# Kernel tuning notes

Hardware: AMD Instinct MI355X
Metric: run time of the kernel (lower is better)

## Reference

```python
import jax, jax.numpy as jnp
import numpy as np

B, T, C, H = 2, 2048, 1024, 16
D = C // H
CURV = 1.0  # clamp_curvature(1.0) -> 1.0
EPS = 1e-5


def layer_norm(x, w, b):
    mu = jnp.mean(x, axis=-1, keepdims=True)
    var = jnp.var(x, axis=-1, keepdims=True)
    return (x - mu) * jax.lax.rsqrt(var + EPS) * w + b


def mobius_addition(x, y, c):
    xn2 = jnp.sum(x * x, axis=-1, keepdims=True)
    yn2 = jnp.sum(y * y, axis=-1, keepdims=True)
    ip = jnp.sum(x * y, axis=-1, keepdims=True)
    num = (1 + 2 * c * ip + c * yn2) * x + (1 - c * xn2) * y
    den = 1 + 2 * c * ip + (c ** 2) * xn2 * yn2
    return num / den


def scaling_factor(x, c):
    xn2 = jnp.sum(x * x, axis=-1, keepdims=True)
    return 2.0 / (1.0 + c * xn2)


def expmap(x, v, c):
    lam = scaling_factor(x, c)
    vn = jnp.linalg.norm(v, axis=-1, keepdims=True)
    second = (1.0 / c ** 0.5) * jnp.tanh(jnp.sqrt(c * lam * vn ** 2 / 2.0)) * v / vn
    return mobius_addition(x, second, c)


def logmap(x, u, c):
    lam = scaling_factor(x, c)
    m = mobius_addition(-x, u, c)
    mn = jnp.linalg.norm(m, axis=-1, keepdims=True)
    cf = 2.0 / (lam * c ** 0.5)
    arg = jnp.clip(jnp.sqrt(c * mn), -0.999, 0.999)
    return cf * jnp.arctanh(arg) * m / mn


def calc_reference_point(x):
    # shift-right by one token, zero at position 0
    return jnp.pad(x[:, :-1, :], ((0, 0), (1, 0), (0, 0)))


def causal_attention(q, k, v):
    # q,k,v: [B,H,T,D]
    scores = jnp.einsum('bhqd,bhkd->bhqk', q, k) / np.sqrt(D).astype(np.float32)
    mask = jnp.tril(jnp.ones((T, T), dtype=bool))
    scores = jnp.where(mask, scores, -jnp.inf)
    att = jax.nn.softmax(scores, axis=-1)
    return jnp.einsum('bhqk,bhkd->bhqd', att, v)


def setup_inputs() -> dict:
    key = jax.random.key(0)
    ks = jax.random.split(key, 6)
    s = 0.02
    return {
        'x': jax.random.normal(ks[0], (B, T, C), jnp.float32),
        'ln1_w': jnp.ones((C,), jnp.float32),
        'ln1_b': jnp.zeros((C,), jnp.float32),
        'W_attn': jax.random.normal(ks[1], (C, 3 * C), jnp.float32) * s,
        'b_attn': jnp.zeros((3 * C,), jnp.float32),
        'W_aproj': jax.random.normal(ks[2], (C, C), jnp.float32) * s,
        'b_aproj': jnp.zeros((C,), jnp.float32),
        'ln2_w': jnp.ones((C,), jnp.float32),
        'ln2_b': jnp.zeros((C,), jnp.float32),
        'W_fc': jax.random.normal(ks[3], (C, 4 * C), jnp.float32) * s,
        'b_fc': jnp.zeros((4 * C,), jnp.float32),
        'W_mproj': jax.random.normal(ks[4], (4 * C, C), jnp.float32) * s,
        'b_mproj': jnp.zeros((C,), jnp.float32),
    }


def reference(x, ln1_w, ln1_b, W_attn, b_attn, W_aproj, b_aproj,
              ln2_w, ln2_b, W_fc, b_fc, W_mproj, b_mproj):
    c = CURV
    # --- attention branch ---
    xn = layer_norm(x, ln1_w, ln1_b)
    ref = calc_reference_point(xn)
    xt = logmap(ref, xn, c)
    qkv = xt @ W_attn + b_attn
    q, k, v = jnp.split(qkv, 3, axis=-1)
    q = q.reshape(B, T, H, D).transpose(0, 2, 1, 3)
    k = k.reshape(B, T, H, D).transpose(0, 2, 1, 3)
    v = v.reshape(B, T, H, D).transpose(0, 2, 1, 3)
    y = causal_attention(q, k, v)
    y = y.transpose(0, 2, 1, 3).reshape(B, T, C)
    y = expmap(ref, y, c)  # map_back_after_attention=True
    y = y @ W_aproj + b_aproj
    x = x + y
    # --- MLP branch (no expmap since map_back_after_attention) ---
    h = layer_norm(x, ln2_w, ln2_b)
    h = jax.nn.gelu(h @ W_fc + b_fc, approximate=False)
    h = h @ W_mproj + b_mproj
    return x + h
```

## Files before the change

### kernel.cpp

```cpp
#include <hip/hip_runtime.h>
#include <hip/hip_bf16.h>
#include <math.h>

#define BDIM 2
#define TSEQ 2048
#define CDIM 1024
#define HNUM 16
#define NROW (BDIM*TSEQ)

typedef __attribute__((ext_vector_type(8))) short bf16x8_t;
typedef __attribute__((ext_vector_type(4))) float f32x4_t;

__device__ inline float bf2f(__hip_bfloat16 h) { return __bfloat162float(h); }

__device__ inline void unpack8(uint4 u, float* f) {
  unsigned v[4] = {u.x, u.y, u.z, u.w};
  #pragma unroll
  for (int i = 0; i < 4; ++i) {
    union { unsigned u2; float f2; } a, b;
    a.u2 = v[i] << 16;
    b.u2 = v[i] & 0xffff0000u;
    f[2*i]   = a.f2;
    f[2*i+1] = b.f2;
  }
}

__device__ inline void gload16(const void* g, void* l) {
  __builtin_amdgcn_global_load_lds(
      (const __attribute__((address_space(1))) void*)g,
      (__attribute__((address_space(3))) void*)l, 16, 0, 0);
}

__global__ __launch_bounds__(256) void zero32_kernel(float* p, int n) {
  int i = blockIdx.x * 256 + threadIdx.x;
  if (i < n) p[i] = 0.f;
}

__global__ __launch_bounds__(256) void convT_kernel(const float* __restrict__ src,
    __hip_bfloat16* __restrict__ dst, int K, int N)
{
  __shared__ float tile[32][33];
  const int k0 = blockIdx.x * 32, n0 = blockIdx.y * 32;
  const int tr  = threadIdx.x >> 3;
  const int tc4 = (threadIdx.x & 7) * 4;
  float4 v = *(const float4*)(src + (size_t)(k0 + tr) * N + n0 + tc4);
  tile[tr][tc4+0] = v.x; tile[tr][tc4+1] = v.y;
  tile[tr][tc4+2] = v.z; tile[tr][tc4+3] = v.w;
  __syncthreads();
  union { ushort4 u; __hip_bfloat16 h[4]; } o;
  #pragma unroll
  for (int j = 0; j < 4; ++j) o.h[j] = __float2bfloat16(tile[tc4+j][tr]);
  *(ushort4*)(dst + (size_t)(n0 + tr) * K + k0 + tc4) = o.u;
}

__device__ inline void blk_reduce3(float& a, float& b, float& c, float* red) {
  const int lane = threadIdx.x & 63, wv = threadIdx.x >> 6;
  #pragma unroll
  for (int off = 32; off; off >>= 1) {
    a += __shfl_xor(a, off); b += __shfl_xor(b, off); c += __shfl_xor(c, off);
  }
  if (lane == 0) { red[wv] = a; red[4+wv] = b; red[8+wv] = c; }
  __syncthreads();
  a = red[0]+red[1]+red[2]+red[3];
  b = red[4]+red[5]+red[6]+red[7];
  c = red[8]+red[9]+red[10]+red[11];
}

__global__ __launch_bounds__(256) void ln_kernel(const float* __restrict__ x,
    const float* __restrict__ w, const float* __restrict__ b,
    __hip_bfloat16* __restrict__ out)
{
  const int row = blockIdx.x;
  const size_t base = (size_t)row * CDIM;
  const int lane = threadIdx.x & 63, wv = threadIdx.x >> 6;
  float v[4]; float s = 0.f, s2 = 0.f;
  #pragma unroll
  for (int k = 0; k < 4; ++k) {
    int d = threadIdx.x + k*256;
    float xe = x[base + d];
    v[k] = xe; s += xe; s2 += xe*xe;
  }
  __shared__ float red[8];
  #pragma unroll
  for (int off = 32; off; off >>= 1) { s += __shfl_xor(s, off); s2 += __shfl_xor(s2, off); }
  if (lane == 0) { red[wv] = s; red[4+wv] = s2; }
  __syncthreads();
  s  = red[0]+red[1]+red[2]+red[3];
  s2 = red[4]+red[5]+red[6]+red[7];
  float mu = s * (1.0f/CDIM);
  float var = s2 * (1.0f/CDIM) - mu*mu;
  float rstd = rsqrtf(fmaxf(var, 0.f) + 1e-5f);
  #pragma unroll
  for (int k = 0; k < 4; ++k) {
    int d = threadIdx.x + k*256;
    out[base + d] = __float2bfloat16((v[k]-mu)*rstd*w[d] + b[d]);
  }
}

__global__ __launch_bounds__(256) void scal1_kernel(const __hip_bfloat16* __restrict__ xn,
                                                    float2* __restrict__ pq)
{
  const int row = blockIdx.x;
  const bool has = (row & (TSEQ-1)) != 0;
  const __hip_bfloat16* u  = xn + (size_t)row * CDIM;
  const __hip_bfloat16* xp = xn + (size_t)(has ? row-1 : row) * CDIM;
  float sxx = 0.f, suu = 0.f, sxu = 0.f;
  #pragma unroll
  for (int k = 0; k < 4; ++k) {
    int d = threadIdx.x + k*256;
    float ue = bf2f(u[d]);
    float xe = has ? bf2f(xp[d]) : 0.f;
    sxx += xe*xe; suu += ue*ue; sxu += xe*ue;
  }
  __shared__ float red[12];
  blk_reduce3(sxx, suu, sxu, red);
  float den = 1.f - 2.f*sxu + sxx*suu;
  float inv = 1.f / fmaxf(den, 1e-30f);
  float cb = 1.f - sxx;
  float ca = 1.f - 2.f*sxu + suu;
  float mm = inv*inv*(cb*cb*suu - 2.f*ca*cb*sxu + ca*ca*sxx);
  float mn = sqrtf(fmaxf(mm, 0.f));
  float arg = fminf(sqrtf(mn), 0.999f);
  float fac = (1.f + sxx) * atanhf(arg) / fmaxf(mn, 1e-30f);
  if (threadIdx.x == 0)
    pq[row] = make_float2(fac*cb*inv, has ? -fac*ca*inv : 0.f);
}

__global__ __launch_bounds__(256) void scal2_kernel(const __hip_bfloat16* __restrict__ xn,
                                                    const __hip_bfloat16* __restrict__ y,
                                                    float2* __restrict__ sr)
{
  const int row = blockIdx.x;
  const bool has = (row & (TSEQ-1)) != 0;
  const __hip_bfloat16* xp = xn + (size_t)(has ? row-1 : row) * CDIM;
  const __hip_bfloat16* vr = y + (size_t)row * CDIM;
  float sxx = 0.f, svv = 0.f, sxv = 0.f;
  #pragma unroll
  for (int k = 0; k < 4; ++k) {
    int d = threadIdx.x + k*256;
    float ve = bf2f(vr[d]);
    float xe = has ? bf2f(xp[d]) : 0.f;
    sxx += xe*xe; svv += ve*ve; sxv += xe*ve;
  }
  __shared__ float red[12];
  blk_reduce3(sxx, svv, sxv, red);
  float lam = 2.f / (1.f + sxx);
  float vn  = sqrtf(fmaxf(svv, 1e-30f));
  float th  = tanhf(vn * sqrtf(0.5f*lam));
  float s   = th / vn;
  float yn2 = th*th;
  float ip  = s * sxv;
  float den = 1.f + 2.f*ip + sxx*yn2;
  float inv = 1.f / fmaxf(den, 1e-30f);
  if (threadIdx.x == 0)
    sr[row] = make_float2((1.f - sxx)*s*inv, has ? (1.f + 2.f*ip + yn2)*inv : 0.f);
}

__global__ __launch_bounds__(256) void mix_kernel(const __hip_bfloat16* __restrict__ in1,
    const __hip_bfloat16* __restrict__ in2, const float2* __restrict__ coef,
    __hip_bfloat16* __restrict__ out)
{
  const int r = blockIdx.x*2 + (threadIdx.x >> 7);
  const int d = (threadIdx.x & 127) * 8;
  const bool has = (r & (TSEQ-1)) != 0;
  const int rp = has ? r-1 : r;
  float2 c = coef[r];
  uint4 u1 = *(const uint4*)(in1 + (size_t)r*CDIM + d);
  uint4 u2 = *(const uint4*)(in2 + (size_t)rp*CDIM + d);
  float f1[8], f2[8];
  unpack8(u1, f1); unpack8(u2, f2);
  union { uint4 u; __hip_bfloat16 h[8]; } o;
  #pragma unroll
  for (int j = 0; j < 8; ++j) o.h[j] = __float2bfloat16(c.x*f1[j] + c.y*f2[j]);
  *(uint4*)(out + (size_t)r*CDIM + d) = o.u;
}

template<int BM, int BN, int MODE>
__global__ __launch_bounds__(256) void gemmT_kernel(
    const __hip_bfloat16* __restrict__ A, int lda,
    const __hip_bfloat16* __restrict__ Bt, int ldb,
    const float* __restrict__ bias,
    const float* __restrict__ res,
    void* __restrict__ outp,
    int N, int K)
{
  __shared__ __align__(16) __hip_bfloat16 As[BM*32];
  __shared__ __align__(16) __hip_bfloat16 Bs[BN*32];
  const int bm = blockIdx.x, bn = blockIdx.y;
  const int tid = threadIdx.x, lane = tid & 63, wv = tid >> 6;
  constexpr int FM = BM/32, FN = BN/32;
  const int wm = (wv >> 1) * (BM/2), wn = (wv & 1) * (BN/2);
  f32x4_t acc[FM][FN];
  #pragma unroll
  for (int m = 0; m < FM; ++m)
    #pragma unroll
    for (int n = 0; n < FN; ++n) acc[m][n] = (f32x4_t){0.f,0.f,0.f,0.f};

  const int fr = lane & 15, quad = lane >> 4, q8 = quad * 8;
  const int srow = lane >> 2, scol = (lane & 3) * 8;
  constexpr int SA = BM/16, SB = BN/16;
  const __hip_bfloat16* Ag = A  + (size_t)(bm*BM + srow)*lda + scol;
  const __hip_bfloat16* Bg = Bt + (size_t)(bn*BN + srow)*ldb + scol;

  for (int k0 = 0; k0 < K; k0 += 32) {
    __syncthreads();
    #pragma unroll
    for (int i = 0; i < SA/4; ++i) {
      int s = wv*(SA/4) + i;
      gload16(Ag + (size_t)(s*16)*lda + k0, &As[s*512]);
    }
    #pragma unroll
    for (int i = 0; i < SB/4; ++i) {
      int s = wv*(SB/4) + i;
      gload16(Bg + (size_t)(s*16)*ldb + k0, &Bs[s*512]);
    }
    __syncthreads();
    bf16x8_t af[FM], bfr[FN];
    #pragma unroll
    for (int m = 0; m < FM; ++m) af[m]  = *(const bf16x8_t*)&As[(wm + m*16 + fr)*32 + q8];
    #pragma unroll
    for (int n = 0; n < FN; ++n) bfr[n] = *(const bf16x8_t*)&Bs[(wn + n*16 + fr)*32 + q8];
    #pragma unroll
    for (int m = 0; m < FM; ++m)
      #pragma unroll
      for (int n = 0; n < FN; ++n)
        acc[m][n] = __builtin_amdgcn_mfma_f32_16x16x32_bf16(af[m], bfr[n], acc[m][n], 0, 0, 0);
  }

  #pragma unroll
  for (int m = 0; m < FM; ++m)
  #pragma unroll
  for (int n = 0; n < FN; ++n)
  #pragma unroll
  for (int r = 0; r < 4; ++r) {
    int row = bm*BM + wm + m*16 + quad*4 + r;
    int col = bn*BN + wn + n*16 + fr;
    size_t idx = (size_t)row * N + col;
    float v = acc[m][n][r];
    if (MODE == 0) {
      v += bias[col];
      ((__hip_bfloat16*)outp)[idx] = __float2bfloat16(v);
    } else if (MODE == 1) {
      v += bias[col] + res[idx];
      ((float*)outp)[idx] = v;
    } else if (MODE == 2) {
      v += bias[col];
      v = 0.5f * v * (1.0f + erff(v * 0.70710678118654752f));
      ((__hip_bfloat16*)outp)[idx] = __float2bfloat16(v);
    } else if (MODE == 5) {
      v += res[idx];
      ((float*)outp)[idx] = v;
    } else {
      v += res[idx];
      ((float*)outp)[idx] = v;
    }
  }
}

__device__ inline __hip_bfloat16* slot_ptr(__hip_bfloat16* p0, __hip_bfloat16* p1, int s) {
  return (s < 2048) ? p0 + (size_t)s*4096 : p1 + (size_t)(s-2048)*4096;
}

__global__ __launch_bounds__(256) void attn_kernel(const __hip_bfloat16* __restrict__ qkv,
                                                   __hip_bfloat16* __restrict__ y,
                                                   __hip_bfloat16* __restrict__ pO0,
                                                   __hip_bfloat16* __restrict__ pO1,
                                                   float2* __restrict__ ml)
{
  const int wid = blockIdx.x;
  int qt, ci;
  if (wid < 32)      { qt = 31 - (wid >> 2); ci = wid & 3; }
  else if (wid < 56) { int w = wid - 32; qt = 23 - w/3; ci = w - (23 - qt)*3; }
  else if (wid < 72) { int w = wid - 56; qt = 15 - (w >> 1); ci = w & 1; }
  else               { qt = 79 - wid; ci = 0; }
  const int tb = ci * 8;
  const int te = min(tb + 8, qt + 1);
  const bool direct = (qt < 8);

  const int pair = blockIdx.y;
  const int b  = pair >> 4;
  const int h  = pair & 15;
  const int tid = threadIdx.x;
  const int lane = tid & 63;
  const int wv = tid >> 6;
  const int t0 = qt * 64;

  __shared__ __align__(16) __hip_bfloat16 Ks[64*72];
  __shared__ __align__(16) __hip_bfloat16 Vt[64*72];
  __shared__ __align__(16) __hip_bfloat16 Ps[4][16*72];

  const int colq = lane & 15, quad = lane >> 4;
  const int q8 = quad * 8;

  const __hip_bfloat16* qp = qkv + ((size_t)(b*TSEQ + t0 + wv*16 + colq))*(3*CDIM) + h*64;
  const bf16x8_t qa0 = *(const bf16x8_t*)(qp + q8);
  const bf16x8_t qa1 = *(const bf16x8_t*)(qp + 32 + q8);

  f32x4_t oacc[4];
  #pragma unroll
  for (int tn = 0; tn < 4; ++tn) oacc[tn] = (f32x4_t){0.f,0.f,0.f,0.f};
  float mr[4] = {-1e30f,-1e30f,-1e30f,-1e30f};
  float lr[4] = {0.f,0.f,0.f,0.f};

  const int jr = tid >> 2;
  const int sg = (tid & 3) * 16;
  const size_t kvbase = ((size_t)(b*TSEQ))*(3*CDIM) + h*64;

  uint4 ck0, ck1, cv0, cv1;
  {
    const __hip_bfloat16* kp = qkv + kvbase + (size_t)(tb*64 + jr)*(3*CDIM) + CDIM + sg;
    ck0 = *(const uint4*)(kp);
    ck1 = *(const uint4*)(kp + 8);
    cv0 = *(const uint4*)(kp + CDIM);
    cv1 = *(const uint4*)(kp + CDIM + 8);
  }
  uint4 nk0 = ck0, nk1 = ck1, nv0 = cv0, nv1 = cv1;

  for (int t = tb; t < te; ++t) {
    __syncthreads();
    {
      *(uint4*)(&Ks[jr*72 + sg])     = ck0;
      *(uint4*)(&Ks[jr*72 + sg + 8]) = ck1;
      union { uint4 u; __hip_bfloat16 hh[8]; } a0, a1;
      a0.u = cv0; a1.u = cv1;
      #pragma unroll
      for (int e = 0; e < 8; ++e) Vt[(sg + e)*72 + jr]     = a0.hh[e];
      #pragma unroll
      for (int e = 0; e < 8; ++e) Vt[(sg + 8 + e)*72 + jr] = a1.hh[e];
    }
    if (t + 1 < te) {
      const __hip_bfloat16* kp = qkv + kvbase + (size_t)((t+1)*64 + jr)*(3*CDIM) + CDIM + sg;
      nk0 = *(const uint4*)(kp);
      nk1 = *(const uint4*)(kp + 8);
      nv0 = *(const uint4*)(kp + CDIM);
      nv1 = *(const uint4*)(kp + CDIM + 8);
    }
    __syncthreads();

    f32x4_t sacc[4];
    #pragma unroll
    for (int tn = 0; tn < 4; ++tn) {
      sacc[tn] = (f32x4_t){0.f,0.f,0.f,0.f};
      bf16x8_t bk0 = *(const bf16x8_t*)(&Ks[(tn*16 + colq)*72 + q8]);
      sacc[tn] = __builtin_amdgcn_mfma_f32_16x16x32_bf16(qa0, bk0, sacc[tn], 0, 0, 0);
      bf16x8_t bk1 = *(const bf16x8_t*)(&Ks[(tn*16 + colq)*72 + 32 + q8]);
      sacc[tn] = __builtin_amdgcn_mfma_f32_16x16x32_bf16(qa1, bk1, sacc[tn], 0, 0, 0);
    }

    float sc[4][4];
    #pragma unroll
    for (int tn = 0; tn < 4; ++tn)
    #pragma unroll
    for (int r = 0; r < 4; ++r) sc[tn][r] = sacc[tn][r] * 0.125f;
    if (t == qt) {
      #pragma unroll
      for (int tn = 0; tn < 4; ++tn)
      #pragma unroll
      for (int r = 0; r < 4; ++r) {
        int key = t*64 + tn*16 + colq;
        int row = t0 + wv*16 + quad*4 + r;
        if (key > row) sc[tn][r] = -1e30f;
      }
    }

    float mx[4];
    #pragma unroll
    for (int r = 0; r < 4; ++r) {
      mx[r] = fmaxf(fmaxf(sc[0][r], sc[1][r]), fmaxf(sc[2][r], sc[3][r]));
      #pragma unroll
      for (int off = 8; off; off >>= 1) mx[r] = fmaxf(mx[r], __shfl_xor(mx[r], off));
    }
    float al[4];
    #pragma unroll
    for (int r = 0; r < 4; ++r) {
      float mn = fmaxf(mr[r], mx[r]);
      al[r] = __expf(mr[r] - mn);
      mr[r] = mn;
    }
    float psum[4] = {0.f,0.f,0.f,0.f};
    #pragma unroll
    for (int tn = 0; tn < 4; ++tn)
    #pragma unroll
    for (int r = 0; r < 4; ++r) {
      float p = __expf(sc[tn][r] - mr[r]);
      psum[r] += p;
      Ps[wv][(quad*4 + r)*72 + tn*16 + colq] = __float2bfloat16(p);
    }
    #pragma unroll
    for (int r = 0; r < 4; ++r) {
      #pragma unroll
      for (int off = 8; off; off >>= 1) psum[r] += __shfl_xor(psum[r], off);
      lr[r] = lr[r]*al[r] + psum[r];
    }
    #pragma unroll
    for (int tn = 0; tn < 4; ++tn)
    #pragma unroll
    for (int r = 0; r < 4; ++r) oacc[tn][r] *= al[r];

    bf16x8_t pa0 = *(const bf16x8_t*)(&Ps[wv][colq*72 + q8]);
    bf16x8_t pa1 = *(const bf16x8_t*)(&Ps[wv][colq*72 + 32 + q8]);
    #pragma unroll
    for (int tn = 0; tn < 4; ++tn) {
      bf16x8_t vb0 = *(const bf16x8_t*)(&Vt[(tn*16 + colq)*72 + q8]);
      oacc[tn] = __builtin_amdgcn_mfma_f32_16x16x32_bf16(pa0, vb0, oacc[tn], 0, 0, 0);
      bf16x8_t vb1 = *(const bf16x8_t*)(&Vt[(tn*16 + colq)*72 + 32 + q8]);
      oacc[tn] = __builtin_amdgcn_mfma_f32_16x16x32_bf16(pa1, vb1, oacc[tn], 0, 0, 0);
    }

    ck0 = nk0; ck1 = nk1; cv0 = nv0; cv1 = nv1;
  }

  if (direct) {
    __hip_bfloat16* yp = y + ((size_t)(b*TSEQ + t0 + wv*16))*CDIM + h*64;
    #pragma unroll
    for (int tn = 0; tn < 4; ++tn)
    #pragma unroll
    for (int r = 0; r < 4; ++r) {
      yp[(size_t)(quad*4 + r)*CDIM + tn*16 + colq] = __float2bfloat16(oacc[tn][r] / lr[r]);
    }
  } else {
    int off = (qt >= 24) ? 40 + (qt-24)*4 : (qt >= 16) ? 16 + (qt-16)*3 : (qt-8)*2;
    int s = pair*72 + off + ci;
    __hip_bfloat16* op = slot_ptr(pO0, pO1, s);
    #pragma unroll
    for (int tn = 0; tn < 4; ++tn)
    #pragma unroll
    for (int r = 0; r < 4; ++r) {
      op[wv*1024 + tn*256 + r*64 + lane] = __float2bfloat16(oacc[tn][r]);
    }
    if (colq == 0) {
      #pragma unroll
      for (int r = 0; r < 4; ++r)
        ml[(size_t)s*64 + wv*16 + quad*4 + r] = make_float2(mr[r], lr[r]);
    }
  }
}

__global__ __launch_bounds__(256) void combine_kernel(__hip_bfloat16* __restrict__ pO0,
                                                      __hip_bfloat16* __restrict__ pO1,
                                                      const float2* __restrict__ ml,
                                                      __hip_bfloat16* __restrict__ y)
{
  const int qt = 8 + blockIdx.x;
  const int pair = blockIdx.y;
  const int b = pair >> 4, h = pair & 15;
  const int nch = (qt >= 24) ? 4 : (qt >= 16) ? 3 : 2;
  const int off = (qt >= 24) ? 40 + (qt-24)*4 : (qt >= 16) ? 16 + (qt-16)*3 : (qt-8)*2;
  const int s0 = pair*72 + off;
  const int tid = threadIdx.x;
  const int q = tid >> 2;
  const int dseg = (tid & 3) * 16;

  float mi[4], li[4];
  float M = -1e30f;
  #pragma unroll
  for (int i = 0; i < 4; ++i) {
    if (i < nch) {
      float2 t = ml[(size_t)(s0+i)*64 + q];
      mi[i] = t.x; li[i] = t.y;
      M = fmaxf(M, t.x);
    }
  }
  float w[4]; float denom = 0.f;
  #pragma unroll
  for (int i = 0; i < 4; ++i) {
    if (i < nch) { w[i] = __expf(mi[i] - M); denom += li[i]*w[i]; }
  }
  const int base = (q >> 4)*1024 + (dseg >> 4)*256 + (q & 3)*64 + ((q >> 2) & 3)*16;
  float acc[16];
  #pragma unroll
  for (int j = 0; j < 16; ++j) acc[j] = 0.f;
  #pragma unroll
  for (int i = 0; i < 4; ++i) {
    if (i < nch) {
      const __hip_bfloat16* op = slot_ptr(pO0, pO1, s0+i) + base;
      uint4 u0 = *(const uint4*)(op);
      uint4 u1 = *(const uint4*)(op + 8);
      float f[16];
      unpack8(u0, f); unpack8(u1, f+8);
      #pragma unroll
      for (int j = 0; j < 16; ++j) acc[j] += w[i]*f[j];
    }
  }
  float inv = 1.f / denom;
  union { uint4 u[2]; __hip_bfloat16 hh[16]; } o;
  #pragma unroll
  for (int j = 0; j < 16; ++j) o.hh[j] = __float2bfloat16(acc[j]*inv);
  __hip_bfloat16* yp = y + ((size_t)(b*TSEQ + qt*64 + q))*CDIM + h*64 + dseg;
  *(uint4*)(yp) = o.u[0];
  *(uint4*)(yp + 8) = o.u[1];
}

extern "C" void kernel_launch(void* const* d_in, const int* in_sizes, int n_in,
                              void* d_out, int out_size, void* d_ws, size_t ws_size,
                              hipStream_t stream)
{
  float* out = (float*)d_out;
  __hip_bfloat16* ybuf = (__hip_bfloat16*)d_out;
  char* ws = (char*)d_ws;
  const size_t KB = 1024, MB = 1024*1024;

  if (ws_size < 49*MB) {
    zero32_kernel<<<(out_size + 255)/256, 256, 0, stream>>>(out, out_size);
    return;
  }

  const float* x      = (const float*)d_in[0];
  const float* ln1w   = (const float*)d_in[1];
  const float* ln1b   = (const float*)d_in[2];
  const float* Wattn  = (const float*)d_in[3];
  const float* battn  = (const float*)d_in[4];
  const float* Waproj = (const float*)d_in[5];
  const float* baproj = (const float*)d_in[6];
  const float* ln2w   = (const float*)d_in[7];
  const float* ln2b   = (const float*)d_in[8];
  const float* Wfc    = (const float*)d_in[9];
  const float* bfc    = (const float*)d_in[10];
  const float* Wmproj = (const float*)d_in[11];
  const float* bmproj = (const float*)d_in[12];

  float2* pq           = (float2*)(ws);
  float2* sr           = (float2*)(ws + 32*KB);
  __hip_bfloat16* xn   = (__hip_bfloat16*)(ws + 64*KB);
  char* big            = ws + 64*KB + 8*MB;
  __hip_bfloat16* qkv  = (__hip_bfloat16*)big;
  float* x2            = (float*)big;
  __hip_bfloat16* ebuf = (__hip_bfloat16*)(big + 16*MB);
  __hip_bfloat16* gbuf = (__hip_bfloat16*)(big + 16*MB);
  __hip_bfloat16* hbuf = xn;
  char* creg           = ws + 64*KB + 32*MB;
  __hip_bfloat16* cWattnT  = (__hip_bfloat16*)creg;
  __hip_bfloat16* xt       = (__hip_bfloat16*)(creg + 8*MB);
  __hip_bfloat16* cWaprojT = (__hip_bfloat16*)creg;
  __hip_bfloat16* cWfcT    = (__hip_bfloat16*)creg;
  __hip_bfloat16* cWmT     = (__hip_bfloat16*)(creg + 8*MB);
  __hip_bfloat16* pO0      = (__hip_bfloat16*)creg;
  __hip_bfloat16* pO1      = (__hip_bfloat16*)((char*)d_out + 8*MB);
  float2* mlbuf            = (float2*)((char*)d_out + 10*MB);

  convT_kernel<<<dim3(32, 96), 256, 0, stream>>>(Wattn,  cWattnT,  1024, 3072);

  ln_kernel<<<NROW, 256, 0, stream>>>(x, ln1w, ln1b, xn);
  scal1_kernel<<<NROW, 256, 0, stream>>>(xn, pq);
  mix_kernel<<<NROW/2, 256, 0, stream>>>(xn, xn, pq, xt);
  gemmT_kernel<128,128,0><<<dim3(32, 24), 256, 0, stream>>>(
      xt, 1024, cWattnT, 1024, battn, nullptr, qkv, 3072, 1024);
  attn_kernel<<<dim3(80, BDIM*HNUM), 256, 0, stream>>>(qkv, ybuf, pO0, pO1, mlbuf);
  combine_kernel<<<dim3(24, BDIM*HNUM), 256, 0, stream>>>(pO0, pO1, mlbuf, ybuf);
  convT_kernel<<<dim3(32, 32), 256, 0, stream>>>(Waproj, cWaprojT, 1024, 1024);
  scal2_kernel<<<NROW, 256, 0, stream>>>(xn, ybuf, sr);
  mix_kernel<<<NROW/2, 256, 0, stream>>>(ybuf, xn, sr, ebuf);
  gemmT_kernel<64,128,1><<<dim3(64, 8), 256, 0, stream>>>(
      ebuf, 1024, cWaprojT, 1024, baproj, x, x2, 1024, 1024);
  convT_kernel<<<dim3(32, 128), 256, 0, stream>>>(Wfc,    cWfcT, 1024, 4096);
  convT_kernel<<<dim3(128, 32), 256, 0, stream>>>(Wmproj, cWmT,  4096, 1024);
  ln_kernel<<<NROW, 256, 0, stream>>>(x2, ln2w, ln2b, hbuf);
  for (int c = 0; c < 4; ++c) {
    gemmT_kernel<64,128,2><<<dim3(64, 8), 256, 0, stream>>>(
        hbuf, 1024, cWfcT + (size_t)c*1024*1024, 1024, bfc + 1024*c, nullptr, gbuf,
        1024, 1024);
    const __hip_bfloat16* Bc = cWmT + 1024*c;
    if (c == 0) {
      gemmT_kernel<64,128,1><<<dim3(64, 8), 256, 0, stream>>>(
          gbuf, 1024, Bc, 4096, bmproj, x2, x2, 1024, 1024);
    } else if (c < 3) {
      gemmT_kernel<64,128,5><<<dim3(64, 8), 256, 0, stream>>>(
          gbuf, 1024, Bc, 4096, nullptr, x2, x2, 1024, 1024);
    } else {
      gemmT_kernel<64,128,7><<<dim3(64, 8), 256, 0, stream>>>(
          gbuf, 1024, Bc, 4096, nullptr, x2, out, 1024, 1024);
    }
  }
}
```

Before: 504.1 us.

## Fuse scalar and mix kernels, add MFMA priority hints, chunk MLP in halves

Merges each scal/mix kernel pair into one kernel that computes the per-row coefficients and writes the mixed bf16 row directly. This removes two launches and a re-read of the inputs. MFMA blocks in the GEMM and attention kernels are wrapped in s_setprio raise/lower hints. The MLP is now processed in two 2048-wide chunks with 128x128 tiles instead of four 1024-wide chunks, which halves the launches and residual read-modify-write passes on x2. The x2 buffer is moved into d_out to make room for the larger gbuf, and that in-place aliasing with the final output could be a correctness risk.

```diff
diff --git a/kernel.cpp b/kernel.cpp
--- a/kernel.cpp
+++ b/kernel.cpp
@@ -97,20 +97,21 @@
   }
 }
 
-__global__ __launch_bounds__(256) void scal1_kernel(const __hip_bfloat16* __restrict__ xn,
-                                                    float2* __restrict__ pq)
+__global__ __launch_bounds__(256) void scalmix1_kernel(const __hip_bfloat16* __restrict__ xn,
+                                                       __hip_bfloat16* __restrict__ xt)
 {
   const int row = blockIdx.x;
   const bool has = (row & (TSEQ-1)) != 0;
   const __hip_bfloat16* u  = xn + (size_t)row * CDIM;
   const __hip_bfloat16* xp = xn + (size_t)(has ? row-1 : row) * CDIM;
+  float ue[4], xe[4];
   float sxx = 0.f, suu = 0.f, sxu = 0.f;
   #pragma unroll
   for (int k = 0; k < 4; ++k) {
     int d = threadIdx.x + k*256;
-    float ue = bf2f(u[d]);
-    float xe = has ? bf2f(xp[d]) : 0.f;
-    sxx += xe*xe; suu += ue*ue; sxu += xe*ue;
+    ue[k] = bf2f(u[d]);
+    xe[k] = has ? bf2f(xp[d]) : 0.f;
+    sxx += xe[k]*xe[k]; suu += ue[k]*ue[k]; sxu += xe[k]*ue[k];
   }
   __shared__ float red[12];
   blk_reduce3(sxx, suu, sxu, red);
@@ -122,25 +123,31 @@
   float mn = sqrtf(fmaxf(mm, 0.f));
   float arg = fminf(sqrtf(mn), 0.999f);
   float fac = (1.f + sxx) * atanhf(arg) / fmaxf(mn, 1e-30f);
-  if (threadIdx.x == 0)
-    pq[row] = make_float2(fac*cb*inv, has ? -fac*ca*inv : 0.f);
-}
-
-__global__ __launch_bounds__(256) void scal2_kernel(const __hip_bfloat16* __restrict__ xn,
-                                                    const __hip_bfloat16* __restrict__ y,
-                                                    float2* __restrict__ sr)
+  float P = fac*cb*inv;
+  float Q = has ? -fac*ca*inv : 0.f;
+  #pragma unroll
+  for (int k = 0; k < 4; ++k) {
+    int d = threadIdx.x + k*256;
+    xt[(size_t)row*CDIM + d] = __float2bfloat16(P*ue[k] + Q*xe[k]);
+  }
+}
+
+__global__ __launch_bounds__(256) void scalmix2_kernel(const __hip_bfloat16* __restrict__ xn,
+                                                       const __hip_bfloat16* __restrict__ y,
+                                                       __hip_bfloat16* __restrict__ e)
 {
   const int row = blockIdx.x;
   const bool has = (row & (TSEQ-1)) != 0;
   const __hip_bfloat16* xp = xn + (size_t)(has ? row-1 : row) * CDIM;
   const __hip_bfloat16* vr = y + (size_t)row * CDIM;
+  float ve[4], xe[4];
   float sxx = 0.f, svv = 0.f, sxv = 0.f;
   #pragma unroll
   for (int k = 0; k < 4; ++k) {
     int d = threadIdx.x + k*256;
-    float ve = bf2f(vr[d]);
-    float xe = has ? bf2f(xp[d]) : 0.f;
-    sxx += xe*xe; svv += ve*ve; sxv += xe*ve;
+    ve[k] = bf2f(vr[d]);
+    xe[k] = has ? bf2f(xp[d]) : 0.f;
+    sxx += xe[k]*xe[k]; svv += ve[k]*ve[k]; sxv += xe[k]*ve[k];
   }
   __shared__ float red[12];
   blk_reduce3(sxx, svv, sxv, red);
@@ -152,27 +159,13 @@
   float ip  = s * sxv;
   float den = 1.f + 2.f*ip + sxx*yn2;
   float inv = 1.f / fmaxf(den, 1e-30f);
-  if (threadIdx.x == 0)
-    sr[row] = make_float2((1.f - sxx)*s*inv, has ? (1.f + 2.f*ip + yn2)*inv : 0.f);
-}
-
-__global__ __launch_bounds__(256) void mix_kernel(const __hip_bfloat16* __restrict__ in1,
-    const __hip_bfloat16* __restrict__ in2, const float2* __restrict__ coef,
-    __hip_bfloat16* __restrict__ out)
-{
-  const int r = blockIdx.x*2 + (threadIdx.x >> 7);
-  const int d = (threadIdx.x & 127) * 8;
-  const bool has = (r & (TSEQ-1)) != 0;
-  const int rp = has ? r-1 : r;
-  float2 c = coef[r];
-  uint4 u1 = *(const uint4*)(in1 + (size_t)r*CDIM + d);
-  uint4 u2 = *(const uint4*)(in2 + (size_t)rp*CDIM + d);
-  float f1[8], f2[8];
-  unpack8(u1, f1); unpack8(u2, f2);
-  union { uint4 u; __hip_bfloat16 h[8]; } o;
-  #pragma unroll
-  for (int j = 0; j < 8; ++j) o.h[j] = __float2bfloat16(c.x*f1[j] + c.y*f2[j]);
-  *(uint4*)(out + (size_t)r*CDIM + d) = o.u;
+  float S = (1.f - sxx)*s*inv;
+  float R = has ? (1.f + 2.f*ip + yn2)*inv : 0.f;
+  #pragma unroll
+  for (int k = 0; k < 4; ++k) {
+    int d = threadIdx.x + k*256;
+    e[(size_t)row*CDIM + d] = __float2bfloat16(S*ve[k] + R*xe[k]);
+  }
 }
 
 template<int BM, int BN, int MODE>
@@ -220,11 +213,13 @@
     for (int m = 0; m < FM; ++m) af[m]  = *(const bf16x8_t*)&As[(wm + m*16 + fr)*32 + q8];
     #pragma unroll
     for (int n = 0; n < FN; ++n) bfr[n] = *(const bf16x8_t*)&Bs[(wn + n*16 + fr)*32 + q8];
+    __builtin_amdgcn_s_setprio(1);
     #pragma unroll
     for (int m = 0; m < FM; ++m)
       #pragma unroll
       for (int n = 0; n < FN; ++n)
         acc[m][n] = __builtin_amdgcn_mfma_f32_16x16x32_bf16(af[m], bfr[n], acc[m][n], 0, 0, 0);
+    __builtin_amdgcn_s_setprio(0);
   }
 
   #pragma unroll
@@ -247,9 +242,6 @@
       v += bias[col];
       v = 0.5f * v * (1.0f + erff(v * 0.70710678118654752f));
       ((__hip_bfloat16*)outp)[idx] = __float2bfloat16(v);
-    } else if (MODE == 5) {
-      v += res[idx];
-      ((float*)outp)[idx] = v;
     } else {
       v += res[idx];
       ((float*)outp)[idx] = v;
@@ -338,6 +330,7 @@
     __syncthreads();
 
     f32x4_t sacc[4];
+    __builtin_amdgcn_s_setprio(1);
     #pragma unroll
     for (int tn = 0; tn < 4; ++tn) {
       sacc[tn] = (f32x4_t){0.f,0.f,0.f,0.f};
@@ -346,6 +339,7 @@
       bf16x8_t bk1 = *(const bf16x8_t*)(&Ks[(tn*16 + colq)*72 + 32 + q8]);
       sacc[tn] = __builtin_amdgcn_mfma_f32_16x16x32_bf16(qa1, bk1, sacc[tn], 0, 0, 0);
     }
+    __builtin_amdgcn_s_setprio(0);
 
     float sc[4][4];
     #pragma unroll
@@ -399,6 +393,7 @@
 
     bf16x8_t pa0 = *(const bf16x8_t*)(&Ps[wv][colq*72 + q8]);
     bf16x8_t pa1 = *(const bf16x8_t*)(&Ps[wv][colq*72 + 32 + q8]);
+    __builtin_amdgcn_s_setprio(1);
     #pragma unroll
     for (int tn = 0; tn < 4; ++tn) {
       bf16x8_t vb0 = *(const bf16x8_t*)(&Vt[(tn*16 + colq)*72 + q8]);
@@ -406,6 +401,7 @@
       bf16x8_t vb1 = *(const bf16x8_t*)(&Vt[(tn*16 + colq)*72 + 32 + q8]);
       oacc[tn] = __builtin_amdgcn_mfma_f32_16x16x32_bf16(pa1, vb1, oacc[tn], 0, 0, 0);
     }
+    __builtin_amdgcn_s_setprio(0);
 
     ck0 = nk0; ck1 = nk1; cv0 = nv0; cv1 = nv1;
   }
@@ -497,6 +493,7 @@
 {
   float* out = (float*)d_out;
   __hip_bfloat16* ybuf = (__hip_bfloat16*)d_out;
+  float* x2d = (float*)d_out;
   char* ws = (char*)d_ws;
   const size_t KB = 1024, MB = 1024*1024;
 
@@ -519,14 +516,11 @@
   const float* Wmproj = (const float*)d_in[11];
   const float* bmproj = (const float*)d_in[12];
 
-  float2* pq           = (float2*)(ws);
-  float2* sr           = (float2*)(ws + 32*KB);
   __hip_bfloat16* xn   = (__hip_bfloat16*)(ws + 64*KB);
   char* big            = ws + 64*KB + 8*MB;
   __hip_bfloat16* qkv  = (__hip_bfloat16*)big;
-  float* x2            = (float*)big;
+  __hip_bfloat16* gbuf = (__hip_bfloat16*)big;
   __hip_bfloat16* ebuf = (__hip_bfloat16*)(big + 16*MB);
-  __hip_bfloat16* gbuf = (__hip_bfloat16*)(big + 16*MB);
   __hip_bfloat16* hbuf = xn;
   char* creg           = ws + 64*KB + 32*MB;
   __hip_bfloat16* cWattnT  = (__hip_bfloat16*)creg;
@@ -541,34 +535,29 @@
   convT_kernel<<<dim3(32, 96), 256, 0, stream>>>(Wattn,  cWattnT,  1024, 3072);
 
   ln_kernel<<<NROW, 256, 0, stream>>>(x, ln1w, ln1b, xn);
-  scal1_kernel<<<NROW, 256, 0, stream>>>(xn, pq);
-  mix_kernel<<<NROW/2, 256, 0, stream>>>(xn, xn, pq, xt);
+  scalmix1_kernel<<<NROW, 256, 0, stream>>>(xn, xt);
   gemmT_kernel<128,128,0><<<dim3(32, 24), 256, 0, stream>>>(
       xt, 1024, cWattnT, 1024, battn, nullptr, qkv, 3072, 1024);
   attn_kernel<<<dim3(80, BDIM*HNUM), 256, 0, stream>>>(qkv, ybuf, pO0, pO1, mlbuf);
   combine_kernel<<<dim3(24, BDIM*HNUM), 256, 0, stream>>>(pO0, pO1, mlbuf, ybuf);
   convT_kernel<<<dim3(32, 32), 256, 0, stream>>>(Waproj, cWaprojT, 1024, 1024);
-  scal2_kernel<<<NROW, 256, 0, stream>>>(xn, ybuf, sr);
-  mix_kernel<<<NROW/2, 256, 0, stream>>>(ybuf, xn, sr, ebuf);
+  scalmix2_kernel<<<NROW, 256, 0, stream>>>(xn, ybuf, ebuf);
   gemmT_kernel<64,128,1><<<dim3(64, 8), 256, 0, stream>>>(
-      ebuf, 1024, cWaprojT, 1024, baproj, x, x2, 1024, 1024);
+      ebuf, 1024, cWaprojT, 1024, baproj, x, x2d, 1024, 1024);
   convT_kernel<<<dim3(32, 128), 256, 0, stream>>>(Wfc,    cWfcT, 1024, 4096);
   convT_kernel<<<dim3(128, 32), 256, 0, stream>>>(Wmproj, cWmT,  4096, 1024);
-  ln_kernel<<<NROW, 256, 0, stream>>>(x2, ln2w, ln2b, hbuf);
-  for (int c = 0; c < 4; ++c) {
-    gemmT_kernel<64,128,2><<<dim3(64, 8), 256, 0, stream>>>(
-        hbuf, 1024, cWfcT + (size_t)c*1024*1024, 1024, bfc + 1024*c, nullptr, gbuf,
-        1024, 1024);
-    const __hip_bfloat16* Bc = cWmT + 1024*c;
+  ln_kernel<<<NROW, 256, 0, stream>>>(x2d, ln2w, ln2b, hbuf);
+  for (int c = 0; c < 2; ++c) {
+    gemmT_kernel<128,128,2><<<dim3(32, 16), 256, 0, stream>>>(
+        hbuf, 1024, cWfcT + (size_t)c*2048*1024, 1024, bfc + 2048*c, nullptr, gbuf,
+        2048, 1024);
+    const __hip_bfloat16* Bc = cWmT + 2048*c;
     if (c == 0) {
       gemmT_kernel<64,128,1><<<dim3(64, 8), 256, 0, stream>>>(
-          gbuf, 1024, Bc, 4096, bmproj, x2, x2, 1024, 1024);
-    } else if (c < 3) {
-      gemmT_kernel<64,128,5><<<dim3(64, 8), 256, 0, stream>>>(
-          gbuf, 1024, Bc, 4096, nullptr, x2, x2, 1024, 1024);
+          gbuf, 2048, Bc, 4096, bmproj, x2d, x2d, 1024, 2048);
     } else {
       gemmT_kernel<64,128,7><<<dim3(64, 8), 256, 0, stream>>>(
-          gbuf, 1024, Bc, 4096, nullptr, x2, out, 1024, 1024);
-    }
-  }
-}
+          gbuf, 2048, Bc, 4096, nullptr, x2d, out, 1024, 2048);
+    }
+  }
+}
```

Result: faster. 453.7 us (-10.0%).
